# Kernel optimization log

Hardware: AMD Instinct MI355X
Metric: run time of the kernel (lower is better)

The kernel has to match this reference:

```python
import jax, jax.numpy as jnp
import numpy as np

NUM_GRAPHS = 16
NODES_PER = 1024
D = 128
H = 2
KPOS = 20
E = 262144


def _ln(x, g, b):
    mu = jnp.mean(x, axis=-1, keepdims=True)
    var = jnp.mean((x - mu) ** 2, axis=-1, keepdims=True)
    return (x - mu) * jax.lax.rsqrt(var + 1e-5) * g + b


def setup_inputs() -> dict:
    key = jax.random.key(0)
    ks = jax.random.split(key, 12)
    N = NUM_GRAPHS * NODES_PER
    s = 0.02
    return {
        "x": jax.random.normal(ks[0], (N, D), jnp.float32),
        "pos_enc": jax.random.normal(ks[1], (N, KPOS), jnp.float32),
        "pe_w": jax.random.normal(ks[2], (D, KPOS), jnp.float32) * s,
        "pe_b": jnp.zeros((D,), jnp.float32),
        "in_w": jax.random.normal(ks[3], (3 * D, D), jnp.float32) * s,
        "in_b": jnp.zeros((3 * D,), jnp.float32),
        "out_w": jax.random.normal(ks[4], (D, D), jnp.float32) * s,
        "out_b": jnp.zeros((D,), jnp.float32),
        "ln1_g": jnp.ones((D,), jnp.float32),
        "ln1_b": jnp.zeros((D,), jnp.float32),
        "ln2_g": jnp.ones((D,), jnp.float32),
        "ln2_b": jnp.zeros((D,), jnp.float32),
        "ff1_w": jax.random.normal(ks[5], (4 * D, D), jnp.float32) * s,
        "ff1_b": jnp.zeros((4 * D,), jnp.float32),
        "ff2_w": jax.random.normal(ks[6], (D, 4 * D), jnp.float32) * s,
        "ff2_b": jnp.zeros((D,), jnp.float32),
        "edge_index": jax.random.randint(ks[7], (2, E), 0, N, dtype=jnp.int32),
        "batch": jnp.repeat(jnp.arange(NUM_GRAPHS, dtype=jnp.int32), NODES_PER),
    }


def reference(x, pos_enc, pe_w, pe_b, in_w, in_b, out_w, out_b,
              ln1_g, ln1_b, ln2_g, ln2_b, ff1_w, ff1_b, ff2_w, ff2_b,
              edge_index, batch):
    # pos_enc Linear + add, then per-graph transformer (graphs equal-sized -> batched)
    h = x + pos_enc @ pe_w.T + pe_b  # (N, D)
    h = h.reshape(NUM_GRAPHS, NODES_PER, D)  # (B, S, D)

    hd = D // H
    qkv = h @ in_w.T + in_b  # (B, S, 3D)
    q, k, v = jnp.split(qkv, 3, axis=-1)

    def heads(t):
        return t.reshape(NUM_GRAPHS, NODES_PER, H, hd).transpose(0, 2, 1, 3)

    q, k, v = heads(q), heads(k), heads(v)  # (B, H, S, hd)
    scores = jnp.einsum('bhqd,bhkd->bhqk', q, k) / jnp.float32(np.sqrt(hd))
    attn = jax.nn.softmax(scores, axis=-1)
    ctx = jnp.einsum('bhqk,bhkd->bhqd', attn, v)
    ctx = ctx.transpose(0, 2, 1, 3).reshape(NUM_GRAPHS, NODES_PER, D)
    sa = ctx @ out_w.T + out_b

    # post-norm (PyTorch TransformerEncoderLayer default, eval mode: no dropout)
    h = _ln(h + sa, ln1_g, ln1_b)
    ff = jax.nn.relu(h @ ff1_w.T + ff1_b) @ ff2_w.T + ff2_b
    h = _ln(h + ff, ln2_g, ln2_b)
    return h.reshape(-1, D)
```

## Files before the change

### kernel.cpp

```cpp
#include <hip/hip_runtime.h>

typedef unsigned short u16;

#define NGRAPH 16
#define SEQ    1024
#define DIM    128
#define NHEAD  2
#define HDIM   64
#define KPOS   20
#define NTOT   (NGRAPH*SEQ)
#define QKVD   (3*DIM)

__device__ __forceinline__ float bf2f(u16 u) {
    return __uint_as_float(((unsigned int)u) << 16);
}
__device__ __forceinline__ u16 f2bf(float f) {
    unsigned int u = __float_as_uint(f);
    u += 0x7fffu + ((u >> 16) & 1u);
    return (u16)(u >> 16);
}

template<int CTRL>
__device__ __forceinline__ float dpp_ror(float x) {
    return __int_as_float(__builtin_amdgcn_update_dpp(
        __float_as_int(x), __float_as_int(x), CTRL, 0xF, 0xF, true));
}
__device__ __forceinline__ float row16_max(float x) {
    x = fmaxf(x, dpp_ror<0x121>(x));
    x = fmaxf(x, dpp_ror<0x122>(x));
    x = fmaxf(x, dpp_ror<0x124>(x));
    x = fmaxf(x, dpp_ror<0x128>(x));
    return x;
}
__device__ __forceinline__ float row16_sum(float x) {
    x += dpp_ror<0x121>(x);
    x += dpp_ror<0x122>(x);
    x += dpp_ror<0x124>(x);
    x += dpp_ror<0x128>(x);
    return x;
}

__device__ __forceinline__ float ld1(const void* p, int fbf, size_t i) {
    return fbf ? bf2f(((const u16*)p)[i]) : ((const float*)p)[i];
}
__device__ __forceinline__ float4 ldw8(const void* W, int fbf, size_t i) {
    if (fbf) return *(const float4*)((const u16*)W + i);
    const float* q = (const float*)W + i;
    float4 a = *(const float4*)q, b = *(const float4*)(q + 4);
    float4 r;
    u16* d = (u16*)&r;
    d[0]=f2bf(a.x); d[1]=f2bf(a.y); d[2]=f2bf(a.z); d[3]=f2bf(a.w);
    d[4]=f2bf(b.x); d[5]=f2bf(b.y); d[6]=f2bf(b.z); d[7]=f2bf(b.w);
    return r;
}
__device__ __forceinline__ void ld8f(const void* p, int fbf, size_t i, float* o) {
    if (fbf) {
        float4 v = *(const float4*)((const u16*)p + i);
        const u16* q = (const u16*)&v;
#pragma unroll
        for (int j = 0; j < 8; ++j) o[j] = bf2f(q[j]);
    } else {
        float4 a = *(const float4*)((const float*)p + i);
        float4 b = *(const float4*)((const float*)p + i + 4);
        o[0]=a.x; o[1]=a.y; o[2]=a.z; o[3]=a.w;
        o[4]=b.x; o[5]=b.y; o[6]=b.z; o[7]=b.w;
    }
}

typedef __attribute__((ext_vector_type(8))) short bf16x8;
typedef __attribute__((ext_vector_type(4))) float f32x4;

__device__ __forceinline__ void gload16(const u16* g, u16* l) {
    __builtin_amdgcn_global_load_lds(
        (const __attribute__((address_space(1))) unsigned int*)(g),
        (__attribute__((address_space(3))) unsigned int*)(l), 16, 0, 0);
}
#define VMCNT0() asm volatile("s_waitcnt vmcnt(0)" ::: "memory")

__device__ __forceinline__ int detect_bf16(const u16* x) {
    int ok = 1;
    for (int i = 0; i < 256; i += 2) {
        unsigned e = (x[i] >> 7) & 0xFF;
        if (e < 60u || e > 180u) ok = 0;
    }
    return ok;
}
__global__ void detect_kernel(const u16* __restrict__ x, int* __restrict__ flag) {
    if (threadIdx.x == 0 && blockIdx.x == 0) *flag = detect_bf16(x);
}

__global__ __launch_bounds__(256)
void wconv_kernel(const void* __restrict__ in_w, const void* __restrict__ out_w,
                  const void* __restrict__ ff1_w, const void* __restrict__ ff2_w,
                  const u16* __restrict__ x,
                  u16* __restrict__ wbf, int* __restrict__ flag) {
    __shared__ int fsh;
    if (threadIdx.x == 0) {
        int ok = detect_bf16(x);
        fsh = ok;
        if (blockIdx.x == 0) *flag = ok;
    }
    __syncthreads();
    int fbf = fsh;
    int i8 = (blockIdx.x * 256 + threadIdx.x) * 8;
    const void* src; int off;
    if      (i8 <  49152) { src = in_w;  off = i8; }
    else if (i8 <  65536) { src = out_w; off = i8 - 49152; }
    else if (i8 < 131072) { src = ff1_w; off = i8 - 65536; }
    else                  { src = ff2_w; off = i8 - 131072; }
    *(float4*)&wbf[i8] = ldw8(src, fbf, off);
}

__global__ __launch_bounds__(256)
void pe_kernel(const void* __restrict__ x, const void* __restrict__ pos,
               const void* __restrict__ pe_w, const void* __restrict__ pe_b,
               u16* __restrict__ h0, const int* __restrict__ flag) {
    int fbf = *flag;
    __shared__ float wsh[DIM][KPOS + 1];
    int t = threadIdx.x;
    for (int i = t; i < DIM * KPOS; i += 256)
        wsh[i / KPOS][i % KPOS] = ld1(pe_w, fbf, i);
    __syncthreads();
    int row = blockIdx.x * 2 + (t >> 7), d = t & 127;
    float acc = 0.f;
#pragma unroll
    for (int k = 0; k < KPOS; ++k)
        acc += ld1(pos, fbf, (size_t)row * KPOS + k) * wsh[d][k];
    int rs = fbf ? 128 : 256;
    h0[(size_t)row * rs + d] =
        f2bf(ld1(x, fbf, (size_t)row * DIM + d) + acc + ld1(pe_b, fbf, d));
}

__global__ __launch_bounds__(256)
void qkvpe_kernel(const void* __restrict__ x, const void* __restrict__ pos,
                  const void* __restrict__ pe_w, const void* __restrict__ pe_b,
                  const u16* __restrict__ W, const void* __restrict__ bias,
                  u16* __restrict__ h0, u16* __restrict__ qkv,
                  u16* __restrict__ vt, const int* __restrict__ flag) {
    int fbf = *flag;
    int rs  = fbf ? 128 : 256;
    __shared__ __align__(16) u16 Ash[64][128];
    __shared__ __align__(16) u16 Wsh[2][128][128];
    __shared__ float wsh[DIM][KPOS + 1];
    __shared__ float possh[64][KPOS + 1];
    int t = threadIdx.x;
    int w = t >> 6, lane = t & 63, l16 = lane & 15, quad = lane >> 4;
    int n0 = blockIdx.x * 64;
    int xr = (l16 & 7) << 3;

#pragma unroll
    for (int i = 0; i < 8; ++i) {
        int r = w * 4 + i * 16 + (lane >> 4);
        int s = (lane & 15) ^ (r & 7);
        gload16(&W[(size_t)r * 128 + s * 8], &Wsh[0][w * 4 + i * 16][0]);
    }
    for (int i = t; i < DIM * KPOS; i += 256)
        wsh[i / KPOS][i % KPOS] = ld1(pe_w, fbf, i);
    for (int i = t; i < 64 * KPOS; i += 256)
        possh[i / KPOS][i % KPOS] =
            ld1(pos, fbf, (size_t)(n0 + i / KPOS) * KPOS + i % KPOS);
    asm volatile("s_waitcnt lgkmcnt(0)" ::: "memory");
    __builtin_amdgcn_s_barrier();

    {
        int g  = t & 15;
        int r0 = t >> 4;
        float acc[4][8];
        float pb[8];
        ld8f(pe_b, fbf, g * 8, pb);
#pragma unroll
        for (int u = 0; u < 4; ++u) {
            int r = r0 + u * 16;
            float xv[8];
            ld8f(x, fbf, (size_t)(n0 + r) * DIM + g * 8, xv);
#pragma unroll
            for (int j = 0; j < 8; ++j) acc[u][j] = xv[j] + pb[j];
        }
#pragma unroll
        for (int k = 0; k < KPOS; ++k) {
            float wk[8], pk[4];
#pragma unroll
            for (int j = 0; j < 8; ++j) wk[j] = wsh[g * 8 + j][k];
#pragma unroll
            for (int u = 0; u < 4; ++u) pk[u] = possh[r0 + u * 16][k];
#pragma unroll
            for (int u = 0; u < 4; ++u)
#pragma unroll
                for (int j = 0; j < 8; ++j) acc[u][j] += pk[u] * wk[j];
        }
#pragma unroll
        for (int u = 0; u < 4; ++u) {
            int r = r0 + u * 16;
            float4 hv; u16* hp = (u16*)&hv;
#pragma unroll
            for (int j = 0; j < 8; ++j) hp[j] = f2bf(acc[u][j]);
            *(float4*)&Ash[r][(g ^ (r & 7)) * 8] = hv;
            *(float4*)&h0[(size_t)(n0 + r) * rs + g * 8] = hv;
        }
    }
    asm volatile("s_waitcnt lgkmcnt(0)" ::: "memory");
    __builtin_amdgcn_s_barrier();

#pragma unroll
    for (int m = 0; m < 3; ++m) {
        int m0 = m * 128;
        if (m < 2) {
#pragma unroll
            for (int i = 0; i < 8; ++i) {
                int r = w * 4 + i * 16 + (lane >> 4);
                int s = (lane & 15) ^ (r & 7);
                gload16(&W[(size_t)(m0 + 128 + r) * 128 + s * 8],
                        &Wsh[(m + 1) & 1][w * 4 + i * 16][0]);
            }
            asm volatile("s_waitcnt vmcnt(8)" ::: "memory");
        } else {
            asm volatile("s_waitcnt vmcnt(0)" ::: "memory");
        }
        __builtin_amdgcn_s_barrier();
        f32x4 acc[8] = {};
        __builtin_amdgcn_s_setprio(1);
#pragma unroll
        for (int kk = 0; kk < 4; ++kk) {
            bf16x8 af = *(const bf16x8*)&Ash[w * 16 + l16][(kk * 32 + quad * 8) ^ xr];
#pragma unroll
            for (int s = 0; s < 8; ++s) {
                bf16x8 bf = *(const bf16x8*)&Wsh[m & 1][s * 16 + l16][(kk * 32 + quad * 8) ^ xr];
                acc[s] = __builtin_amdgcn_mfma_f32_16x16x32_bf16(af, bf, acc[s], 0, 0, 0);
            }
        }
        __builtin_amdgcn_s_setprio(0);
        float bb[8];
#pragma unroll
        for (int s = 0; s < 8; ++s) bb[s] = ld1(bias, fbf, m0 + s * 16 + l16);
#pragma unroll
        for (int r = 0; r < 4; ++r) {
            int lr = w * 16 + quad * 4 + r;
            if (m == 2) {
                int n = n0 + lr;
                int bg = n >> 10, nl = n & 1023;
#pragma unroll
                for (int s = 0; s < 8; ++s)
                    vt[((size_t)(bg * 128) + s * 16 + l16) * SEQ + nl] =
                        f2bf(acc[s][r] + bb[s]);
            } else {
#pragma unroll
                for (int s = 0; s < 8; ++s)
                    qkv[(size_t)(n0 + lr) * QKVD + m0 + s * 16 + l16] =
                        f2bf(acc[s][r] + bb[s]);
            }
        }
        if (m < 2) __builtin_amdgcn_s_barrier();
    }
}

__global__ __launch_bounds__(256)
void attn2_kernel(const u16* __restrict__ qkv, const u16* __restrict__ vtp,
                  u16* __restrict__ ctx) {
    __shared__ __align__(16) u16 Qsh[64][72];
    __shared__ __align__(16) u16 Ksh[2][64][64];
    __shared__ __align__(16) u16 Vsh[2][64][64];
    __shared__ u16 Psh[64][76];
    int t    = threadIdx.x;
    int w    = t >> 6;
    int lane = t & 63;
    int l16  = lane & 15;
    int quad = lane >> 4;
    int xr   = (l16 & 7) << 3;
    int L = blockIdx.x;
    int ngh = gridDim.x >> 4;
    int qt, gh;
    if (ngh >= 8) {
        int g8 = L & 7; int rest = L >> 3;
        qt = rest & 15; gh = (rest >> 4) * 8 + g8;
    } else {
        qt = L & 15; gh = L >> 4;
    }
    int b = gh >> 1, h = gh & 1;

#pragma unroll
    for (int i = 0; i < 2; ++i) {
        int idx = t + i * 256;
        int r = idx >> 3, d8 = (idx & 7) * 8;
        size_t n = (size_t)b * SEQ + qt * 64 + r;
        float4 qv = *(const float4*)&qkv[n * QKVD + h * HDIM + d8];
        u16* qp = (u16*)&qv;
#pragma unroll
        for (int j = 0; j < 8; ++j) qp[j] = f2bf(bf2f(qp[j]) * 0.125f);
        *(float4*)&Qsh[r][d8] = qv;
    }

    const u16* kbase = qkv + (size_t)b * SEQ * QKVD + DIM + h * HDIM;
    const u16* vbase = vtp + (size_t)((b * 2 + h) * 64) * SEQ;

    auto stageKV = [&](int kt, int bf) {
#pragma unroll
        for (int i = 0; i < 2; ++i) {
            int r = w * 8 + i * 32 + (lane >> 3);
            int s = (lane & 7) ^ (r & 7);
            gload16(&kbase[(size_t)(kt * 64 + r) * QKVD + s * 8],
                    &Ksh[bf][w * 8 + i * 32][0]);
        }
#pragma unroll
        for (int i = 0; i < 2; ++i) {
            int r = w * 8 + i * 32 + (lane >> 3);
            int s = (lane & 7) ^ (r & 7);
            gload16(&vbase[(size_t)r * SEQ + kt * 64 + s * 8],
                    &Vsh[bf][w * 8 + i * 32][0]);
        }
    };

    stageKV(0, 0);
    VMCNT0();
    __syncthreads();
    bf16x8 qa0 = *(const bf16x8*)&Qsh[w * 16 + l16][quad * 8];
    bf16x8 qa1 = *(const bf16x8*)&Qsh[w * 16 + l16][32 + quad * 8];

    f32x4 o[4] = {};
    float mrow[4] = {-1e30f, -1e30f, -1e30f, -1e30f};
    float lrow[4] = {};

#pragma unroll 1
    for (int kt = 0; kt < SEQ / 64; ++kt) {
        int cur = kt & 1;
        if (kt + 1 < SEQ / 64) stageKV(kt + 1, cur ^ 1);

        float sc[4][4];
        __builtin_amdgcn_s_setprio(1);
#pragma unroll
        for (int c = 0; c < 4; ++c) {
            bf16x8 kb0 = *(const bf16x8*)&Ksh[cur][c * 16 + l16][(quad * 8) ^ xr];
            bf16x8 kb1 = *(const bf16x8*)&Ksh[cur][c * 16 + l16][(32 + quad * 8) ^ xr];
            f32x4 s = {};
            s = __builtin_amdgcn_mfma_f32_16x16x32_bf16(qa0, kb0, s, 0, 0, 0);
            s = __builtin_amdgcn_mfma_f32_16x16x32_bf16(qa1, kb1, s, 0, 0, 0);
#pragma unroll
            for (int r = 0; r < 4; ++r) sc[c][r] = s[r];
        }
        __builtin_amdgcn_s_setprio(0);
        float alpha[4];
#pragma unroll
        for (int r = 0; r < 4; ++r) {
            float mx = fmaxf(fmaxf(sc[0][r], sc[1][r]), fmaxf(sc[2][r], sc[3][r]));
            mx = row16_max(mx);
            float mnew = fmaxf(mrow[r], mx);
            alpha[r] = __expf(mrow[r] - mnew);
            mrow[r] = mnew;
            float sum = 0.f;
#pragma unroll
            for (int c = 0; c < 4; ++c) {
                float p = __expf(sc[c][r] - mnew);
                sc[c][r] = p;
                sum += p;
            }
            sum = row16_sum(sum);
            lrow[r] = lrow[r] * alpha[r] + sum;
        }
#pragma unroll
        for (int c = 0; c < 4; ++c)
#pragma unroll
            for (int r = 0; r < 4; ++r)
                Psh[w * 16 + quad * 4 + r][c * 16 + l16] = f2bf(sc[c][r]);
#pragma unroll
        for (int dt = 0; dt < 4; ++dt)
#pragma unroll
            for (int r = 0; r < 4; ++r) o[dt][r] *= alpha[r];
        bf16x8 pa0 = *(const bf16x8*)&Psh[w * 16 + l16][quad * 8];
        bf16x8 pa1 = *(const bf16x8*)&Psh[w * 16 + l16][32 + quad * 8];
        __builtin_amdgcn_s_setprio(1);
#pragma unroll
        for (int dt = 0; dt < 4; ++dt) {
            bf16x8 vb0 = *(const bf16x8*)&Vsh[cur][dt * 16 + l16][(quad * 8) ^ xr];
            bf16x8 vb1 = *(const bf16x8*)&Vsh[cur][dt * 16 + l16][(32 + quad * 8) ^ xr];
            o[dt] = __builtin_amdgcn_mfma_f32_16x16x32_bf16(pa0, vb0, o[dt], 0, 0, 0);
            o[dt] = __builtin_amdgcn_mfma_f32_16x16x32_bf16(pa1, vb1, o[dt], 0, 0, 0);
        }
        __builtin_amdgcn_s_setprio(0);
        if (kt + 1 < SEQ / 64) {
            VMCNT0();
            __syncthreads();
        }
    }
#pragma unroll
    for (int r = 0; r < 4; ++r) {
        float inv = 1.f / lrow[r];
        size_t n = (size_t)b * SEQ + qt * 64 + w * 16 + quad * 4 + r;
#pragma unroll
        for (int dt = 0; dt < 4; ++dt)
            ctx[n * DIM + h * HDIM + dt * 16 + l16] = f2bf(o[dt][r] * inv);
    }
}

__global__ __launch_bounds__(256)
void outffn_kernel(const u16* __restrict__ ctx, const u16* __restrict__ Wout,
                   const void* __restrict__ out_b,
                   const void* __restrict__ l1g, const void* __restrict__ l1b,
                   const u16* __restrict__ h0,
                   const u16* __restrict__ W1, const u16* __restrict__ W2,
                   const void* __restrict__ b1, const void* __restrict__ b2,
                   const void* __restrict__ l2g, const void* __restrict__ l2b,
                   void* __restrict__ outp, const int* __restrict__ flag) {
    int fbf = *flag;
    int rs  = fbf ? 128 : 256;
    __shared__ __align__(16) u16 Ash[64][128];
    __shared__ __align__(16) u16 Wsh[2][128][128];
    __shared__ __align__(16) u16 F1sh[4][64][128];
    u16 (*CtxSh)[128]  = (u16(*)[128])&F1sh[0][0][0];
    u16 (*H0Sh)[128]   = (u16(*)[128])&F1sh[1][0][0];
    u16 (*WoutSh)[128] = (u16(*)[128])&F1sh[2][0][0];
    int t = threadIdx.x;
    int w = t >> 6, lane = t & 63, l16 = lane & 15, quad = lane >> 4;
    int n0 = blockIdx.x * 64;
    int xr = (l16 & 7) << 3;

#pragma unroll
    for (int i = 0; i < 4; ++i) {
        int r = w * 4 + i * 16 + (lane >> 4);
        int s = (lane & 15) ^ (r & 7);
        gload16(&ctx[(size_t)(n0 + r) * DIM + s * 8], &CtxSh[w * 4 + i * 16][0]);
    }
#pragma unroll
    for (int i = 0; i < 8; ++i) {
        int r = w * 4 + i * 16 + (lane >> 4);
        int s = (lane & 15) ^ (r & 7);
        gload16(&Wout[(size_t)r * 128 + s * 8], &WoutSh[w * 4 + i * 16][0]);
    }
#pragma unroll
    for (int i = 0; i < 4; ++i) {
        int r = w * 4 + i * 16 + (lane >> 4);
        int s = (lane & 15) ^ (r & 7);
        gload16(&h0[(size_t)(n0 + r) * rs + s * 8], &H0Sh[w * 4 + i * 16][0]);
    }
#pragma unroll
    for (int i = 0; i < 8; ++i) {
        int r = w * 4 + i * 16 + (lane >> 4);
        int s = (lane & 15) ^ (r & 7);
        gload16(&W1[(size_t)r * 128 + s * 8], &Wsh[0][w * 4 + i * 16][0]);
    }
    asm volatile("s_waitcnt vmcnt(8)" ::: "memory");
    __builtin_amdgcn_s_barrier();

    {
        f32x4 acc[8] = {};
        __builtin_amdgcn_s_setprio(1);
#pragma unroll
        for (int kk = 0; kk < 4; ++kk) {
            bf16x8 af = *(const bf16x8*)&CtxSh[w * 16 + l16][(kk * 32 + quad * 8) ^ xr];
#pragma unroll
            for (int s = 0; s < 8; ++s) {
                bf16x8 bf = *(const bf16x8*)&WoutSh[s * 16 + l16][(kk * 32 + quad * 8) ^ xr];
                acc[s] = __builtin_amdgcn_mfma_f32_16x16x32_bf16(af, bf, acc[s], 0, 0, 0);
            }
        }
        __builtin_amdgcn_s_setprio(0);
        float bb[8], gg[8], be[8];
#pragma unroll
        for (int s = 0; s < 8; ++s) {
            bb[s] = ld1(out_b, fbf, s * 16 + l16);
            gg[s] = ld1(l1g, fbf, s * 16 + l16);
            be[s] = ld1(l1b, fbf, s * 16 + l16);
        }
#pragma unroll
        for (int r = 0; r < 4; ++r) {
            int lr = w * 16 + quad * 4 + r;
            float v[8];
#pragma unroll
            for (int s = 0; s < 8; ++s) {
                int e = s * 16 + l16;
                int g = e >> 3;
                float resid = bf2f(H0Sh[lr][((g ^ (lr & 7)) << 3) + (e & 7)]);
                v[s] = acc[s][r] + bb[s] + resid;
            }
            float sm = 0.f, sq = 0.f;
#pragma unroll
            for (int s = 0; s < 8; ++s) { sm += v[s]; sq += v[s] * v[s]; }
            sm = row16_sum(sm);
            sq = row16_sum(sq);
            float mu  = sm * (1.f / DIM);
            float var = fmaxf(sq * (1.f / DIM) - mu * mu, 0.f);
            float rsq = rsqrtf(var + 1e-5f);
#pragma unroll
            for (int s = 0; s < 8; ++s) {
                int e = s * 16 + l16;
                int g = e >> 3;
                Ash[lr][((g ^ (lr & 7)) << 3) + (e & 7)] =
                    f2bf((v[s] - mu) * rsq * gg[s] + be[s]);
            }
        }
        asm volatile("s_waitcnt lgkmcnt(0)" ::: "memory");
        __builtin_amdgcn_s_barrier();
    }

#pragma unroll
    for (int m = 0; m < 4; ++m) {
#pragma unroll
        for (int i = 0; i < 8; ++i) {
            int r = w * 4 + i * 16 + (lane >> 4);
            int s = (lane & 15) ^ (r & 7);
            if (m < 3)
                gload16(&W1[(size_t)((m + 1) * 128 + r) * 128 + s * 8],
                        &Wsh[(m + 1) & 1][w * 4 + i * 16][0]);
            else
                gload16(&W2[(size_t)r * 512 + s * 8],
                        &Wsh[0][w * 4 + i * 16][0]);
        }
        asm volatile("s_waitcnt vmcnt(8)" ::: "memory");
        __builtin_amdgcn_s_barrier();
        f32x4 acc[8] = {};
        __builtin_amdgcn_s_setprio(1);
#pragma unroll
        for (int kk = 0; kk < 4; ++kk) {
            bf16x8 af = *(const bf16x8*)&Ash[w * 16 + l16][(kk * 32 + quad * 8) ^ xr];
#pragma unroll
            for (int s = 0; s < 8; ++s) {
                bf16x8 bf = *(const bf16x8*)&Wsh[m & 1][s * 16 + l16][(kk * 32 + quad * 8) ^ xr];
                acc[s] = __builtin_amdgcn_mfma_f32_16x16x32_bf16(af, bf, acc[s], 0, 0, 0);
            }
        }
        __builtin_amdgcn_s_setprio(0);
        float bb[8];
#pragma unroll
        for (int s = 0; s < 8; ++s) bb[s] = ld1(b1, fbf, m * 128 + s * 16 + l16);
#pragma unroll
        for (int r = 0; r < 4; ++r) {
            int lr = w * 16 + quad * 4 + r;
#pragma unroll
            for (int s = 0; s < 8; ++s) {
                int g = s * 2 + (l16 >> 3);
                F1sh[m][lr][((g ^ (lr & 7)) << 3) + (l16 & 7)] =
                    f2bf(fmaxf(acc[s][r] + bb[s], 0.f));
            }
        }
        asm volatile("s_waitcnt lgkmcnt(0)" ::: "memory");
        __builtin_amdgcn_s_barrier();
    }

    f32x4 acc2[8] = {};
#pragma unroll
    for (int c = 0; c < 4; ++c) {
        if (c < 3) {
#pragma unroll
            for (int i = 0; i < 8; ++i) {
                int r = w * 4 + i * 16 + (lane >> 4);
                int s = (lane & 15) ^ (r & 7);
                gload16(&W2[(size_t)r * 512 + (c + 1) * 128 + s * 8],
                        &Wsh[(c + 1) & 1][w * 4 + i * 16][0]);
            }
            asm volatile("s_waitcnt vmcnt(8)" ::: "memory");
        } else {
            asm volatile("s_waitcnt vmcnt(0)" ::: "memory");
        }
        __builtin_amdgcn_s_barrier();
        __builtin_amdgcn_s_setprio(1);
#pragma unroll
        for (int kk = 0; kk < 4; ++kk) {
            bf16x8 af = *(const bf16x8*)&F1sh[c][w * 16 + l16][(kk * 32 + quad * 8) ^ xr];
#pragma unroll
            for (int s = 0; s < 8; ++s) {
                bf16x8 bf = *(const bf16x8*)&Wsh[c & 1][s * 16 + l16][(kk * 32 + quad * 8) ^ xr];
                acc2[s] = __builtin_amdgcn_mfma_f32_16x16x32_bf16(af, bf, acc2[s], 0, 0, 0);
            }
        }
        __builtin_amdgcn_s_setprio(0);
        if (c < 3) __builtin_amdgcn_s_barrier();
    }

    float bb[8], gg[8], be[8];
#pragma unroll
    for (int s = 0; s < 8; ++s) {
        bb[s] = ld1(b2, fbf, s * 16 + l16);
        gg[s] = ld1(l2g, fbf, s * 16 + l16);
        be[s] = ld1(l2b, fbf, s * 16 + l16);
    }
#pragma unroll
    for (int r = 0; r < 4; ++r) {
        int lr = w * 16 + quad * 4 + r;
        size_t rg = (size_t)(n0 + lr);
        float v[8];
#pragma unroll
        for (int s = 0; s < 8; ++s) {
            int g = s * 2 + (l16 >> 3);
            float resid = bf2f(Ash[lr][((g ^ (lr & 7)) << 3) + (l16 & 7)]);
            v[s] = acc2[s][r] + bb[s] + resid;
        }
        float sm = 0.f, sq = 0.f;
#pragma unroll
        for (int s = 0; s < 8; ++s) { sm += v[s]; sq += v[s] * v[s]; }
        sm = row16_sum(sm);
        sq = row16_sum(sq);
        float mu  = sm * (1.f / DIM);
        float var = fmaxf(sq * (1.f / DIM) - mu * mu, 0.f);
        float rsq = rsqrtf(var + 1e-5f);
        if (fbf) {
            u16* o = (u16*)outp;
#pragma unroll
            for (int s = 0; s < 8; ++s)
                o[rg * 128 + s * 16 + l16] =
                    f2bf((v[s] - mu) * rsq * gg[s] + be[s]);
        } else {
            float* o = (float*)outp;
#pragma unroll
            for (int s = 0; s < 8; ++s)
                o[rg * 128 + s * 16 + l16] =
                    (v[s] - mu) * rsq * gg[s] + be[s];
        }
    }
}

template<int EPI, int NK>
__global__ __launch_bounds__(256)
void mgemm_kernel(const u16* __restrict__ A, const void* __restrict__ W,
                  int wbf16, const void* __restrict__ bias,
                  const u16* __restrict__ resid,
                  const void* __restrict__ lng, const void* __restrict__ lnb,
                  void* __restrict__ outp, u16* __restrict__ vt,
                  int Mtot, int AstrIn,
                  int arow0, int orow0, const int* __restrict__ flag) {
    const int K = NK * 128;
    int fbf  = *flag;
    int wfmt = wbf16 ? 1 : fbf;
    int rs   = fbf ? 128 : 256;
    int Astr = (AstrIn < 0) ? rs : AstrIn;
    __shared__ u16 Ash[64][136];
    __shared__ u16 Wsh[128][136];
    int t = threadIdx.x;
    int w = t >> 6, lane = t & 63, l16 = lane & 15, quad = lane >> 4;
    int n0 = blockIdx.x * 64;
    int m0 = blockIdx.y * 128;
    f32x4 acc[8] = {};
    float4 aR[4], wR[8];
#pragma unroll
    for (int i = 0; i < 4; ++i) {
        int idx = t + i * 256;
        int row = idx >> 4, k8 = (idx & 15) * 8;
        aR[i] = *(const float4*)&A[(size_t)(arow0 + n0 + row) * Astr + k8];
    }
#pragma unroll
    for (int i = 0; i < 8; ++i) {
        int idx = t + i * 256;
        int row = idx >> 4, k8 = (idx & 15) * 8;
        wR[i] = ldw8(W, wfmt, (size_t)(m0 + row) * K + k8);
    }
#pragma unroll 1
    for (int c = 0; c < NK; ++c) {
#pragma unroll
        for (int i = 0; i < 4; ++i) {
            int idx = t + i * 256;
            *(float4*)&Ash[idx >> 4][(idx & 15) * 8] = aR[i];
        }
#pragma unroll
        for (int i = 0; i < 8; ++i) {
            int idx = t + i * 256;
            *(float4*)&Wsh[idx >> 4][(idx & 15) * 8] = wR[i];
        }
        __syncthreads();
        if (c + 1 < NK) {
            int kc = (c + 1) * 128;
#pragma unroll
            for (int i = 0; i < 4; ++i) {
                int idx = t + i * 256;
                int row = idx >> 4, k8 = (idx & 15) * 8;
                aR[i] = *(const float4*)&A[(size_t)(arow0 + n0 + row) * Astr + kc + k8];
            }
#pragma unroll
            for (int i = 0; i < 8; ++i) {
                int idx = t + i * 256;
                int row = idx >> 4, k8 = (idx & 15) * 8;
                wR[i] = ldw8(W, wfmt, (size_t)(m0 + row) * K + kc + k8);
            }
        }
        __builtin_amdgcn_s_setprio(1);
#pragma unroll
        for (int kk = 0; kk < 4; ++kk) {
            bf16x8 af = *(const bf16x8*)&Ash[w * 16 + l16][kk * 32 + quad * 8];
#pragma unroll
            for (int s = 0; s < 8; ++s) {
                bf16x8 bf = *(const bf16x8*)&Wsh[s * 16 + l16][kk * 32 + quad * 8];
                acc[s] = __builtin_amdgcn_mfma_f32_16x16x32_bf16(af, bf, acc[s], 0, 0, 0);
            }
        }
        __builtin_amdgcn_s_setprio(0);
        if (c + 1 < NK) __syncthreads();
    }
    float bb[8];
#pragma unroll
    for (int s = 0; s < 8; ++s) bb[s] = ld1(bias, fbf, m0 + s * 16 + l16);
    float gg[8], be[8];
    if (EPI >= 2) {
#pragma unroll
        for (int s = 0; s < 8; ++s) {
            gg[s] = ld1(lng, fbf, s * 16 + l16);
            be[s] = ld1(lnb, fbf, s * 16 + l16);
        }
    }
#pragma unroll
    for (int r = 0; r < 4; ++r) {
        int lr = w * 16 + quad * 4 + r;
        float v[8];
#pragma unroll
        for (int s = 0; s < 8; ++s) {
            v[s] = acc[s][r] + bb[s];
            if (EPI == 1) v[s] = fmaxf(v[s], 0.f);
        }
        if (EPI <= 1) {
            u16* o = (u16*)outp;
#pragma unroll
            for (int s = 0; s < 8; ++s)
                o[(size_t)(n0 + lr) * Mtot + m0 + s * 16 + l16] = f2bf(v[s]);
        } else {
            size_t rg = (size_t)(orow0 + n0 + lr);
#pragma unroll
            for (int s = 0; s < 8; ++s)
                v[s] += bf2f(resid[rg * rs + s * 16 + l16]);
            float sm = 0.f, sq = 0.f;
#pragma unroll
            for (int s = 0; s < 8; ++s) { sm += v[s]; sq += v[s] * v[s]; }
            sm = row16_sum(sm);
            sq = row16_sum(sq);
            float mu  = sm * (1.f / DIM);
            float var = fmaxf(sq * (1.f / DIM) - mu * mu, 0.f);
            float rsq = rsqrtf(var + 1e-5f);
            if (EPI == 2) {
                u16* o = (u16*)outp;
#pragma unroll
                for (int s = 0; s < 8; ++s)
                    o[rg * rs + s * 16 + l16] =
                        f2bf((v[s] - mu) * rsq * gg[s] + be[s]);
            } else {
                if (fbf) {
                    u16* o = (u16*)outp;
#pragma unroll
                    for (int s = 0; s < 8; ++s)
                        o[rg * 128 + s * 16 + l16] =
                            f2bf((v[s] - mu) * rsq * gg[s] + be[s]);
                } else {
                    float* o = (float*)outp;
#pragma unroll
                    for (int s = 0; s < 8; ++s)
                        o[rg * 128 + s * 16 + l16] =
                            (v[s] - mu) * rsq * gg[s] + be[s];
                }
            }
        }
    }
}

__global__ __launch_bounds__(256)
void attn_lds_kernel(const u16* __restrict__ qkv, u16* __restrict__ ctx) {
    __shared__ u16 Qsh[64][72];
    __shared__ u16 Ksh[64][72];
    __shared__ u16 VshT[64][72];
    __shared__ u16 Psh[64][72];
    int t    = threadIdx.x;
    int w    = t >> 6;
    int lane = t & 63;
    int l16  = lane & 15;
    int quad = lane >> 4;
    int L = blockIdx.x;
    int qt = L & 15, gh = L >> 4;
    int b = gh >> 1, h = gh & 1;

#pragma unroll
    for (int i = 0; i < 2; ++i) {
        int idx = t + i * 256;
        int r = idx >> 3, d8 = (idx & 7) * 8;
        size_t n = (size_t)b * SEQ + qt * 64 + r;
        float4 qv = *(const float4*)&qkv[n * QKVD + h * HDIM + d8];
        u16* qp = (u16*)&qv;
#pragma unroll
        for (int j = 0; j < 8; ++j) qp[j] = f2bf(bf2f(qp[j]) * 0.125f);
        *(float4*)&Qsh[r][d8] = qv;
    }
    int kr = t >> 3, kd8 = (t & 7) * 8;
    int vr = t & 63, vdb = (t >> 6) * 16;
    float4 kR[2], vR[2];
    {
        size_t nk0 = (size_t)b * SEQ + kr;
        kR[0] = *(const float4*)&qkv[nk0 * QKVD + DIM + h * HDIM + kd8];
        kR[1] = *(const float4*)&qkv[(nk0 + 32) * QKVD + DIM + h * HDIM + kd8];
        size_t nv0 = (size_t)b * SEQ + vr;
        vR[0] = *(const float4*)&qkv[nv0 * QKVD + 2 * DIM + h * HDIM + vdb];
        vR[1] = *(const float4*)&qkv[nv0 * QKVD + 2 * DIM + h * HDIM + vdb + 8];
    }
    __syncthreads();
    bf16x8 qa0 = *(const bf16x8*)&Qsh[w * 16 + l16][quad * 8];
    bf16x8 qa1 = *(const bf16x8*)&Qsh[w * 16 + l16][32 + quad * 8];

    f32x4 o[4] = {};
    float mrow[4] = {-1e30f, -1e30f, -1e30f, -1e30f};
    float lrow[4] = {};

#pragma unroll 1
    for (int kt = 0; kt < SEQ / 64; ++kt) {
        *(float4*)&Ksh[kr][kd8]      = kR[0];
        *(float4*)&Ksh[kr + 32][kd8] = kR[1];
        {
            const u16* pa = (const u16*)&vR[0];
            const u16* pb = (const u16*)&vR[1];
#pragma unroll
            for (int j = 0; j < 8; ++j) VshT[vdb + j][vr] = pa[j];
#pragma unroll
            for (int j = 0; j < 8; ++j) VshT[vdb + 8 + j][vr] = pb[j];
        }
        __syncthreads();
        if (kt + 1 < SEQ / 64) {
            size_t nk0 = (size_t)b * SEQ + (kt + 1) * 64 + kr;
            kR[0] = *(const float4*)&qkv[nk0 * QKVD + DIM + h * HDIM + kd8];
            kR[1] = *(const float4*)&qkv[(nk0 + 32) * QKVD + DIM + h * HDIM + kd8];
            size_t nv0 = (size_t)b * SEQ + (kt + 1) * 64 + vr;
            vR[0] = *(const float4*)&qkv[nv0 * QKVD + 2 * DIM + h * HDIM + vdb];
            vR[1] = *(const float4*)&qkv[nv0 * QKVD + 2 * DIM + h * HDIM + vdb + 8];
        }
        float sc[4][4];
        __builtin_amdgcn_s_setprio(1);
#pragma unroll
        for (int c = 0; c < 4; ++c) {
            bf16x8 kb0 = *(const bf16x8*)&Ksh[c * 16 + l16][quad * 8];
            bf16x8 kb1 = *(const bf16x8*)&Ksh[c * 16 + l16][32 + quad * 8];
            f32x4 s = {};
            s = __builtin_amdgcn_mfma_f32_16x16x32_bf16(qa0, kb0, s, 0, 0, 0);
            s = __builtin_amdgcn_mfma_f32_16x16x32_bf16(qa1, kb1, s, 0, 0, 0);
#pragma unroll
            for (int r = 0; r < 4; ++r) sc[c][r] = s[r];
        }
        __builtin_amdgcn_s_setprio(0);
        float alpha[4];
#pragma unroll
        for (int r = 0; r < 4; ++r) {
            float mx = fmaxf(fmaxf(sc[0][r], sc[1][r]), fmaxf(sc[2][r], sc[3][r]));
            mx = row16_max(mx);
            float mnew = fmaxf(mrow[r], mx);
            alpha[r] = __expf(mrow[r] - mnew);
            mrow[r] = mnew;
            float sum = 0.f;
#pragma unroll
            for (int c = 0; c < 4; ++c) {
                float p = __expf(sc[c][r] - mnew);
                sc[c][r] = p;
                sum += p;
            }
            sum = row16_sum(sum);
            lrow[r] = lrow[r] * alpha[r] + sum;
        }
#pragma unroll
        for (int c = 0; c < 4; ++c)
#pragma unroll
            for (int r = 0; r < 4; ++r)
                Psh[w * 16 + quad * 4 + r][c * 16 + l16] = f2bf(sc[c][r]);
#pragma unroll
        for (int dt = 0; dt < 4; ++dt)
#pragma unroll
            for (int r = 0; r < 4; ++r) o[dt][r] *= alpha[r];
        bf16x8 pa0 = *(const bf16x8*)&Psh[w * 16 + l16][quad * 8];
        bf16x8 pa1 = *(const bf16x8*)&Psh[w * 16 + l16][32 + quad * 8];
        __builtin_amdgcn_s_setprio(1);
#pragma unroll
        for (int dt = 0; dt < 4; ++dt) {
            bf16x8 vb0 = *(const bf16x8*)&VshT[dt * 16 + l16][quad * 8];
            bf16x8 vb1 = *(const bf16x8*)&VshT[dt * 16 + l16][32 + quad * 8];
            o[dt] = __builtin_amdgcn_mfma_f32_16x16x32_bf16(pa0, vb0, o[dt], 0, 0, 0);
            o[dt] = __builtin_amdgcn_mfma_f32_16x16x32_bf16(pa1, vb1, o[dt], 0, 0, 0);
        }
        __builtin_amdgcn_s_setprio(0);
        __syncthreads();
    }
#pragma unroll
    for (int r = 0; r < 4; ++r) {
        float inv = 1.f / lrow[r];
        size_t n = (size_t)b * SEQ + qt * 64 + w * 16 + quad * 4 + r;
#pragma unroll
        for (int dt = 0; dt < 4; ++dt)
            ctx[n * DIM + h * HDIM + dt * 16 + l16] = f2bf(o[dt][r] * inv);
    }
}

extern "C" void kernel_launch(void* const* d_in, const int* in_sizes, int n_in,
                              void* d_out, int out_size, void* d_ws, size_t ws_size,
                              hipStream_t stream) {
    const void* x     = d_in[0];
    const void* pos   = d_in[1];
    const void* pe_w  = d_in[2];
    const void* pe_b  = d_in[3];
    const void* in_w  = d_in[4];
    const void* in_b  = d_in[5];
    const void* out_w = d_in[6];
    const void* out_b = d_in[7];
    const void* ln1_g = d_in[8];
    const void* ln1_b = d_in[9];
    const void* ln2_g = d_in[10];
    const void* ln2_b = d_in[11];
    const void* ff1_w = d_in[12];
    const void* ff1_b = d_in[13];
    const void* ff2_w = d_in[14];
    const void* ff2_b = d_in[15];

    char* wsb  = (char*)d_ws;
    int*  flag = (int*)(wsb + ((ws_size - 4) & ~(size_t)3));
    u16*  h01  = (u16*)d_out;
    const size_t MB = 1024 * 1024;

    if (ws_size >= 21 * MB) {
        u16* qkv = (u16*)wsb;
        u16* ctx = (u16*)(wsb + 12 * MB);
        u16* vt  = (u16*)(wsb + 16 * MB);
        u16* wbf = (u16*)(wsb + 20 * MB);
        u16* wb_in  = wbf;
        u16* wb_out = wbf + 49152;
        u16* wb_ff1 = wbf + 65536;
        u16* wb_ff2 = wbf + 131072;

        wconv_kernel<<<96, 256, 0, stream>>>(in_w, out_w, ff1_w, ff2_w,
                                             (const u16*)x, wbf, flag);
        qkvpe_kernel<<<NTOT / 64, 256, 0, stream>>>(
            x, pos, pe_w, pe_b, wb_in, in_b, h01, qkv, vt, flag);
        attn2_kernel<<<NGRAPH * NHEAD * 16, 256, 0, stream>>>(qkv, vt, ctx);
        outffn_kernel<<<NTOT / 64, 256, 0, stream>>>(
            ctx, wb_out, out_b, ln1_g, ln1_b, h01,
            wb_ff1, wb_ff2, ff1_b, ff2_b, ln2_g, ln2_b, d_out, flag);
    } else {
        u16* qkv_g = (u16*)wsb;
        u16* ctx_g = (u16*)(wsb + 768 * 1024);
        u16* f1_g  = (u16*)wsb;
        detect_kernel<<<1, 1, 0, stream>>>((const u16*)x, flag);
        pe_kernel<<<NTOT / 2, 256, 0, stream>>>(x, pos, pe_w, pe_b, h01, flag);
        for (int g = 0; g < NGRAPH; ++g) {
            int row0 = g * SEQ;
            mgemm_kernel<0,1><<<dim3(SEQ / 64, 3), 256, 0, stream>>>(
                h01, in_w, 0, in_b, nullptr, nullptr, nullptr, qkv_g, nullptr,
                QKVD, -1, row0, 0, flag);
            attn_lds_kernel<<<NHEAD * 16, 256, 0, stream>>>(qkv_g, ctx_g);
            mgemm_kernel<2,1><<<dim3(SEQ / 64, 1), 256, 0, stream>>>(
                ctx_g, out_w, 0, out_b, h01, ln1_g, ln1_b, h01, nullptr,
                DIM, DIM, 0, row0, flag);
        }
        for (int g = 0; g < NGRAPH; ++g) {
            int row0 = g * SEQ;
            mgemm_kernel<1,1><<<dim3(SEQ / 64, 4), 256, 0, stream>>>(
                h01, ff1_w, 0, ff1_b, nullptr, nullptr, nullptr, f1_g, nullptr,
                4 * DIM, -1, row0, 0, flag);
            mgemm_kernel<3,4><<<dim3(SEQ / 64, 1), 256, 0, stream>>>(
                f1_g, ff2_w, 0, ff2_b, h01, ln2_g, ln2_b, d_out, nullptr,
                DIM, 4 * DIM, 0, row0, flag);
        }
    }
}
```

Before: 169.9 us.

## Interleave FFN1/FFN2 in 64-wide chunks with triple-buffered LDS to cut shared memory

Restructures the fused out-proj+FFN kernel so the hidden layer is produced and consumed in 64-column chunks: each chunk of ReLU(W1) output is immediately multiplied into the FFN2 accumulator instead of materializing the full 64x512 intermediate. Weight tiles shrink to 16KB and rotate through a three-slot LDS ring, cutting shared memory from about 112KB to 80KB per block so more blocks can be resident per CU. The trade-off is twice as many barriers and smaller MFMA batches per sync point, plus a serial unroll-1 loop.

```diff
diff --git a/kernel.cpp b/kernel.cpp
--- a/kernel.cpp
+++ b/kernel.cpp
@@ -402,11 +402,8 @@
     int fbf = *flag;
     int rs  = fbf ? 128 : 256;
     __shared__ __align__(16) u16 Ash[64][128];
-    __shared__ __align__(16) u16 Wsh[2][128][128];
-    __shared__ __align__(16) u16 F1sh[4][64][128];
-    u16 (*CtxSh)[128]  = (u16(*)[128])&F1sh[0][0][0];
-    u16 (*H0Sh)[128]   = (u16(*)[128])&F1sh[1][0][0];
-    u16 (*WoutSh)[128] = (u16(*)[128])&F1sh[2][0][0];
+    __shared__ __align__(16) u16 Buf[32768];
+    u16* F1 = &Buf[3 * 8192];
     int t = threadIdx.x;
     int w = t >> 6, lane = t & 63, l16 = lane & 15, quad = lane >> 4;
     int n0 = blockIdx.x * 64;
@@ -416,27 +413,23 @@
     for (int i = 0; i < 4; ++i) {
         int r = w * 4 + i * 16 + (lane >> 4);
         int s = (lane & 15) ^ (r & 7);
-        gload16(&ctx[(size_t)(n0 + r) * DIM + s * 8], &CtxSh[w * 4 + i * 16][0]);
+        gload16(&ctx[(size_t)(n0 + r) * DIM + s * 8], &Buf[(w * 4 + i * 16) * 128]);
     }
 #pragma unroll
     for (int i = 0; i < 8; ++i) {
         int r = w * 4 + i * 16 + (lane >> 4);
         int s = (lane & 15) ^ (r & 7);
-        gload16(&Wout[(size_t)r * 128 + s * 8], &WoutSh[w * 4 + i * 16][0]);
+        gload16(&Wout[(size_t)r * 128 + s * 8],
+                &Buf[16384 + (w * 4 + i * 16) * 128]);
     }
 #pragma unroll
     for (int i = 0; i < 4; ++i) {
         int r = w * 4 + i * 16 + (lane >> 4);
         int s = (lane & 15) ^ (r & 7);
-        gload16(&h0[(size_t)(n0 + r) * rs + s * 8], &H0Sh[w * 4 + i * 16][0]);
-    }
-#pragma unroll
-    for (int i = 0; i < 8; ++i) {
-        int r = w * 4 + i * 16 + (lane >> 4);
-        int s = (lane & 15) ^ (r & 7);
-        gload16(&W1[(size_t)r * 128 + s * 8], &Wsh[0][w * 4 + i * 16][0]);
-    }
-    asm volatile("s_waitcnt vmcnt(8)" ::: "memory");
+        gload16(&h0[(size_t)(n0 + r) * rs + s * 8],
+                &Buf[8192 + (w * 4 + i * 16) * 128]);
+    }
+    VMCNT0();
     __builtin_amdgcn_s_barrier();
 
     {
@@ -444,10 +437,10 @@
         __builtin_amdgcn_s_setprio(1);
 #pragma unroll
         for (int kk = 0; kk < 4; ++kk) {
-            bf16x8 af = *(const bf16x8*)&CtxSh[w * 16 + l16][(kk * 32 + quad * 8) ^ xr];
+            bf16x8 af = *(const bf16x8*)&Buf[(w * 16 + l16) * 128 + ((kk * 32 + quad * 8) ^ xr)];
 #pragma unroll
             for (int s = 0; s < 8; ++s) {
-                bf16x8 bf = *(const bf16x8*)&WoutSh[s * 16 + l16][(kk * 32 + quad * 8) ^ xr];
+                bf16x8 bf = *(const bf16x8*)&Buf[16384 + (s * 16 + l16) * 128 + ((kk * 32 + quad * 8) ^ xr)];
                 acc[s] = __builtin_amdgcn_mfma_f32_16x16x32_bf16(af, bf, acc[s], 0, 0, 0);
             }
         }
@@ -467,7 +460,7 @@
             for (int s = 0; s < 8; ++s) {
                 int e = s * 16 + l16;
                 int g = e >> 3;
-                float resid = bf2f(H0Sh[lr][((g ^ (lr & 7)) << 3) + (e & 7)]);
+                float resid = bf2f(Buf[8192 + lr * 128 + ((g ^ (lr & 7)) << 3) + (e & 7)]);
                 v[s] = acc[s][r] + bb[s] + resid;
             }
             float sm = 0.f, sq = 0.f;
@@ -490,78 +483,95 @@
         __builtin_amdgcn_s_barrier();
     }
 
-#pragma unroll
-    for (int m = 0; m < 4; ++m) {
-#pragma unroll
-        for (int i = 0; i < 8; ++i) {
+    auto issueW1 = [&](int mm, int slot) {
+        u16* dst = &Buf[slot * 8192];
+#pragma unroll
+        for (int i = 0; i < 4; ++i) {
             int r = w * 4 + i * 16 + (lane >> 4);
             int s = (lane & 15) ^ (r & 7);
-            if (m < 3)
-                gload16(&W1[(size_t)((m + 1) * 128 + r) * 128 + s * 8],
-                        &Wsh[(m + 1) & 1][w * 4 + i * 16][0]);
-            else
-                gload16(&W2[(size_t)r * 512 + s * 8],
-                        &Wsh[0][w * 4 + i * 16][0]);
-        }
-        asm volatile("s_waitcnt vmcnt(8)" ::: "memory");
+            gload16(&W1[(size_t)(mm * 64 + r) * 128 + s * 8],
+                    &dst[(w * 4 + i * 16) * 128]);
+        }
+    };
+    auto issueW2 = [&](int cc, int slot) {
+        u16* dst = &Buf[slot * 8192];
+#pragma unroll
+        for (int i = 0; i < 4; ++i) {
+            int r = w * 8 + i * 32 + (lane >> 3);
+            int s = (lane & 7) ^ (r & 7);
+            gload16(&W2[(size_t)r * 512 + cc * 64 + s * 8],
+                    &dst[(w * 8 + i * 32) * 64]);
+        }
+    };
+
+    issueW1(0, 0);
+    issueW2(0, 1);
+
+    f32x4 acc2[8] = {};
+#pragma unroll 1
+    for (int m = 0; m < 8; ++m) {
+        int tE = 2 * m, tO = 2 * m + 1;
+        if (m < 7) {
+            issueW1(m + 1, (tE + 2) % 3);
+            asm volatile("s_waitcnt vmcnt(8)" ::: "memory");
+        } else {
+            asm volatile("s_waitcnt vmcnt(4)" ::: "memory");
+        }
         __builtin_amdgcn_s_barrier();
-        f32x4 acc[8] = {};
-        __builtin_amdgcn_s_setprio(1);
-#pragma unroll
-        for (int kk = 0; kk < 4; ++kk) {
-            bf16x8 af = *(const bf16x8*)&Ash[w * 16 + l16][(kk * 32 + quad * 8) ^ xr];
-#pragma unroll
-            for (int s = 0; s < 8; ++s) {
-                bf16x8 bf = *(const bf16x8*)&Wsh[m & 1][s * 16 + l16][(kk * 32 + quad * 8) ^ xr];
-                acc[s] = __builtin_amdgcn_mfma_f32_16x16x32_bf16(af, bf, acc[s], 0, 0, 0);
-            }
-        }
-        __builtin_amdgcn_s_setprio(0);
-        float bb[8];
-#pragma unroll
-        for (int s = 0; s < 8; ++s) bb[s] = ld1(b1, fbf, m * 128 + s * 16 + l16);
-#pragma unroll
-        for (int r = 0; r < 4; ++r) {
-            int lr = w * 16 + quad * 4 + r;
-#pragma unroll
-            for (int s = 0; s < 8; ++s) {
-                int g = s * 2 + (l16 >> 3);
-                F1sh[m][lr][((g ^ (lr & 7)) << 3) + (l16 & 7)] =
-                    f2bf(fmaxf(acc[s][r] + bb[s], 0.f));
+        {
+            const u16* Wt = &Buf[(tE % 3) * 8192];
+            f32x4 a1[4] = {};
+            __builtin_amdgcn_s_setprio(1);
+#pragma unroll
+            for (int kk = 0; kk < 4; ++kk) {
+                bf16x8 af = *(const bf16x8*)&Ash[w * 16 + l16][(kk * 32 + quad * 8) ^ xr];
+#pragma unroll
+                for (int s2 = 0; s2 < 4; ++s2) {
+                    bf16x8 bf = *(const bf16x8*)&Wt[(s2 * 16 + l16) * 128 + ((kk * 32 + quad * 8) ^ xr)];
+                    a1[s2] = __builtin_amdgcn_mfma_f32_16x16x32_bf16(af, bf, a1[s2], 0, 0, 0);
+                }
+            }
+            __builtin_amdgcn_s_setprio(0);
+            float bb[4];
+#pragma unroll
+            for (int s2 = 0; s2 < 4; ++s2)
+                bb[s2] = ld1(b1, fbf, m * 64 + s2 * 16 + l16);
+#pragma unroll
+            for (int r = 0; r < 4; ++r) {
+                int lr = w * 16 + quad * 4 + r;
+#pragma unroll
+                for (int s2 = 0; s2 < 4; ++s2) {
+                    int e = s2 * 16 + l16;
+                    int g = e >> 3;
+                    F1[lr * 64 + ((g ^ (lr & 7)) << 3) + (e & 7)] =
+                        f2bf(fmaxf(a1[s2][r] + bb[s2], 0.f));
+                }
             }
         }
         asm volatile("s_waitcnt lgkmcnt(0)" ::: "memory");
         __builtin_amdgcn_s_barrier();
-    }
-
-    f32x4 acc2[8] = {};
-#pragma unroll
-    for (int c = 0; c < 4; ++c) {
-        if (c < 3) {
-#pragma unroll
-            for (int i = 0; i < 8; ++i) {
-                int r = w * 4 + i * 16 + (lane >> 4);
-                int s = (lane & 15) ^ (r & 7);
-                gload16(&W2[(size_t)r * 512 + (c + 1) * 128 + s * 8],
-                        &Wsh[(c + 1) & 1][w * 4 + i * 16][0]);
-            }
+        if (m < 7) {
+            issueW2(m + 1, (tO + 2) % 3);
             asm volatile("s_waitcnt vmcnt(8)" ::: "memory");
         } else {
             asm volatile("s_waitcnt vmcnt(0)" ::: "memory");
         }
         __builtin_amdgcn_s_barrier();
-        __builtin_amdgcn_s_setprio(1);
-#pragma unroll
-        for (int kk = 0; kk < 4; ++kk) {
-            bf16x8 af = *(const bf16x8*)&F1sh[c][w * 16 + l16][(kk * 32 + quad * 8) ^ xr];
-#pragma unroll
-            for (int s = 0; s < 8; ++s) {
-                bf16x8 bf = *(const bf16x8*)&Wsh[c & 1][s * 16 + l16][(kk * 32 + quad * 8) ^ xr];
-                acc2[s] = __builtin_amdgcn_mfma_f32_16x16x32_bf16(af, bf, acc2[s], 0, 0, 0);
-            }
-        }
-        __builtin_amdgcn_s_setprio(0);
-        if (c < 3) __builtin_amdgcn_s_barrier();
+        {
+            const u16* Wt = &Buf[(tO % 3) * 8192];
+            __builtin_amdgcn_s_setprio(1);
+#pragma unroll
+            for (int kk = 0; kk < 2; ++kk) {
+                bf16x8 af = *(const bf16x8*)&F1[(w * 16 + l16) * 64 + ((kk * 32 + quad * 8) ^ xr)];
+#pragma unroll
+                for (int s = 0; s < 8; ++s) {
+                    bf16x8 bf = *(const bf16x8*)&Wt[(s * 16 + l16) * 64 + ((kk * 32 + quad * 8) ^ xr)];
+                    acc2[s] = __builtin_amdgcn_mfma_f32_16x16x32_bf16(af, bf, acc2[s], 0, 0, 0);
+                }
+            }
+            __builtin_amdgcn_s_setprio(0);
+        }
+        __builtin_amdgcn_s_barrier();
     }
 
     float bb[8], gg[8], be[8];
```

Measured after the change: 172.5 us. No clear change (+1.5%).
